# Optimization experiments

Measured on AMD Instinct MI355X. Metric: run time of the kernel, lower is better.

The kernel has to match this reference:

```python
import jax, jax.numpy as jnp
import numpy as np

D = 8  # polynomial degree; with bias present, basis has D columns (P1..PD)


def setup_inputs() -> dict:
    key = jax.random.key(0)
    k1, k2 = jax.random.split(key)
    batch, n_in, n_out = 65536, 256, 64
    x = jax.random.normal(k1, (batch, n_in), dtype=jnp.float32)
    c_basis = jax.random.normal(k2, (n_out, n_in, D), dtype=jnp.float32) * (1.0 / np.sqrt(n_in * D))
    bias = jnp.zeros((n_out,), dtype=jnp.float32)
    return {"x": x, "c_basis": c_basis, "bias": bias}


def _legendre_basis(x):
    # x: (batch, n_in). Returns (batch, n_in, D) = [P1(t), ..., PD(t)], t = tanh(x).
    t = jnp.tanh(x)
    p_prev = jnp.ones_like(t)  # P0
    p_curr = t                 # P1
    polys = [p_curr]
    for k in range(2, D + 1):  # small fixed-length loop over degree
        p_next = ((2 * k - 1) * t * p_curr - (k - 1) * p_prev) / k
        polys.append(p_next)
        p_prev, p_curr = p_curr, p_next
    return jnp.stack(polys, axis=-1)  # (batch, n_in, D)


def reference(x, c_basis, bias):
    # basis: (batch, n_in, D); contract over (n_in, D) with c_basis (n_out, n_in, D)
    leg = _legendre_basis(x)
    y = jnp.einsum('bid,oid->bo', leg, c_basis)
    return y + bias
```

## Files before the change

kernel.cpp:

```cpp
#include <hip/hip_runtime.h>
#include <hip/hip_bf16.h>

typedef _Float16 half2v __attribute__((ext_vector_type(2)));
typedef _Float16 half8  __attribute__((ext_vector_type(8)));
typedef __attribute__((ext_vector_type(4))) float floatx4;
typedef __attribute__((ext_vector_type(4))) unsigned int uintx4;

#define GLOBAL_AS __attribute__((address_space(1)))
#define LDS_AS __attribute__((address_space(3)))

__device__ __forceinline__ void async_ld16(const void* g, void* l) {
  __builtin_amdgcn_global_load_lds((const GLOBAL_AS unsigned int*)g,
                                   (LDS_AS unsigned int*)l, 16, 0, 0);
}

__device__ __forceinline__ half2v h2(float v) {
  return (half2v){(_Float16)v, (_Float16)v};
}

__device__ __forceinline__ void legendre2_f16(float xv0, float xv1,
                                              half8* fa0, half8* fa1) {
  float e0 = __builtin_amdgcn_exp2f(xv0 * 2.885390081777927f);
  float t0 = 1.0f - 2.0f * __builtin_amdgcn_rcpf(e0 + 1.0f);
  float e1 = __builtin_amdgcn_exp2f(xv1 * 2.885390081777927f);
  float t1 = 1.0f - 2.0f * __builtin_amdgcn_rcpf(e1 + 1.0f);
  half2v t;
  { auto tt = __builtin_amdgcn_cvt_pkrtz(t0, t1); __builtin_memcpy(&t, &tt, 4); }
  half2v p1 = t;
  half2v u2 = t * p1, w2 = u2 - h2(1.0f);  half2v p2 = h2(0.5f)      * w2 + u2;
  half2v u3 = t * p2, w3 = u3 - p1;        half2v p3 = h2(2.0f/3.0f) * w3 + u3;
  half2v u4 = t * p3, w4 = u4 - p2;        half2v p4 = h2(0.75f)     * w4 + u4;
  half2v u5 = t * p4, w5 = u5 - p3;        half2v p5 = h2(0.8f)      * w5 + u5;
  half2v u6 = t * p5, w6 = u6 - p4;        half2v p6 = h2(5.0f/6.0f) * w6 + u6;
  half2v u7 = t * p6, w7 = u7 - p5;        half2v p7 = h2(6.0f/7.0f) * w7 + u7;
  half2v u8 = t * p7, w8 = u8 - p6;        half2v p8 = h2(7.0f/8.0f) * w8 + u8;
  unsigned P[8];
  __builtin_memcpy(&P[0], &p1, 4); __builtin_memcpy(&P[1], &p2, 4);
  __builtin_memcpy(&P[2], &p3, 4); __builtin_memcpy(&P[3], &p4, 4);
  __builtin_memcpy(&P[4], &p5, 4); __builtin_memcpy(&P[5], &p6, 4);
  __builtin_memcpy(&P[6], &p7, 4); __builtin_memcpy(&P[7], &p8, 4);
  union { unsigned u[4]; half8 h; } a0, a1;
#pragma unroll
  for (int j = 0; j < 4; ++j) {
    a0.u[j] = __builtin_amdgcn_perm(P[2*j+1], P[2*j], 0x05040100u);
    a1.u[j] = __builtin_amdgcn_perm(P[2*j+1], P[2*j], 0x07060302u);
  }
  *fa0 = a0.h;
  *fa1 = a1.h;
}

__global__ void conv_kernel(const float* __restrict__ cb, _Float16* __restrict__ ws) {
  int t = blockIdx.x * 128 + threadIdx.x;
  int o = t >> 8;
  int i = t & 255;
  const floatx4* s = (const floatx4*)(cb + ((size_t)o * 256 + i) * 8);
  floatx4 v0 = s[0], v1 = s[1];
  union { _Float16 h[8]; uintx4 u; } w;
  w.h[0] = (_Float16)v0.x; w.h[1] = (_Float16)v0.y;
  w.h[2] = (_Float16)v0.z; w.h[3] = (_Float16)v0.w;
  w.h[4] = (_Float16)v1.x; w.h[5] = (_Float16)v1.y;
  w.h[6] = (_Float16)v1.z; w.h[7] = (_Float16)v1.w;
  *(uintx4*)(ws + (size_t)i * 512 + o * 8) = w.u;
}

#define MB 64
#define NCH 16

__global__ __launch_bounds__(128, 2) void kan_kernel(
    const float* __restrict__ x, const _Float16* __restrict__ ws,
    const float* __restrict__ bias, float* __restrict__ y) {
  __shared__ __align__(16) _Float16 bt[2][16 * 64 * 8];
  __shared__ __align__(16) float xs[2][MB * 16];

  const int tid  = threadIdx.x;
  const int wid  = tid >> 6;
  const int lane = tid & 63;
  const int m    = lane & 15;
  const int q    = lane >> 4;
  const int row_block = blockIdx.x * MB;

  floatx4 acc[2][4];
#pragma unroll
  for (int a = 0; a < 2; ++a)
#pragma unroll
    for (int nt = 0; nt < 4; ++nt) acc[a][nt] = (floatx4){0.f, 0.f, 0.f, 0.f};

  const _Float16* bsrc[8];
#pragma unroll
  for (int t = 0; t < 8; ++t)
    bsrc[t] = ws + (size_t)(t * 128 + wid * 64 + lane) * 8;
  const float* xsrc[2];
#pragma unroll
  for (int t = 0; t < 2; ++t) {
    int slot = t * 128 + wid * 64 + lane;
    int r = slot >> 2;
    int c4 = (slot & 3) ^ (r & 3);
    xsrc[t] = x + (size_t)(row_block + r) * 256 + c4 * 4;
  }

  auto stage = [&](int buf) {
#pragma unroll
    for (int t = 0; t < 8; ++t) {
      int sb = t * 128 + wid * 64;
      async_ld16(bsrc[t], &bt[buf][sb * 8]);
      bsrc[t] += 8192;
    }
#pragma unroll
    for (int t = 0; t < 2; ++t) {
      int sb = t * 128 + wid * 64;
      async_ld16(xsrc[t], &xs[buf][sb * 4]);
      xsrc[t] += 16;
    }
  };

  const int xoff0 = (wid * 32 + m) * 64 + ((m & 3) << 4) + q * 4;
  const int xoff1 = xoff0 + 1024;

  stage(0);
#pragma unroll 2
  for (int ch = 0; ch < NCH; ++ch) {
    const int buf = ch & 1;
    asm volatile("s_barrier" ::: "memory");
    if (ch + 1 < NCH) {
      stage(buf ^ 1);
      asm volatile("s_waitcnt vmcnt(10)" ::: "memory");
    } else {
      asm volatile("s_waitcnt vmcnt(0)" ::: "memory");
    }
    asm volatile("s_barrier" ::: "memory");

    const _Float16* bp = &bt[buf][q * 512 + m * 8];
    const char* xb = (const char*)&xs[buf][0];
#pragma unroll
    for (int ks = 0; ks < 4; ++ks) {
      half8 fb0 = *(const half8*)(bp + ks * 2048 + 0 * 128);
      half8 fb1 = *(const half8*)(bp + ks * 2048 + 1 * 128);
      half8 fb2 = *(const half8*)(bp + ks * 2048 + 2 * 128);
      half8 fb3 = *(const half8*)(bp + ks * 2048 + 3 * 128);
      float xv0 = *(const float*)(xb + (xoff0 ^ (ks << 4)));
      float xv1 = *(const float*)(xb + (xoff1 ^ (ks << 4)));
      half8 fa0, fa1;
      legendre2_f16(xv0, xv1, &fa0, &fa1);
      acc[0][0] = __builtin_amdgcn_mfma_f32_16x16x32_f16(fa0, fb0, acc[0][0], 0, 0, 0);
      acc[1][0] = __builtin_amdgcn_mfma_f32_16x16x32_f16(fa1, fb0, acc[1][0], 0, 0, 0);
      acc[0][1] = __builtin_amdgcn_mfma_f32_16x16x32_f16(fa0, fb1, acc[0][1], 0, 0, 0);
      acc[1][1] = __builtin_amdgcn_mfma_f32_16x16x32_f16(fa1, fb1, acc[1][1], 0, 0, 0);
      acc[0][2] = __builtin_amdgcn_mfma_f32_16x16x32_f16(fa0, fb2, acc[0][2], 0, 0, 0);
      acc[1][2] = __builtin_amdgcn_mfma_f32_16x16x32_f16(fa1, fb2, acc[1][2], 0, 0, 0);
      acc[0][3] = __builtin_amdgcn_mfma_f32_16x16x32_f16(fa0, fb3, acc[0][3], 0, 0, 0);
      acc[1][3] = __builtin_amdgcn_mfma_f32_16x16x32_f16(fa1, fb3, acc[1][3], 0, 0, 0);
    }
  }

  float bv[4];
#pragma unroll
  for (int nt = 0; nt < 4; ++nt) bv[nt] = bias[nt * 16 + m];
#pragma unroll
  for (int a = 0; a < 2; ++a) {
    int gr0 = row_block + wid * 32 + a * 16 + q * 4;
#pragma unroll
    for (int nt = 0; nt < 4; ++nt) {
#pragma unroll
      for (int r = 0; r < 4; ++r) {
        y[(size_t)(gr0 + r) * 64 + nt * 16 + m] = acc[a][nt][r] + bv[nt];
      }
    }
  }
}

extern "C" void kernel_launch(void* const* d_in, const int* in_sizes, int n_in,
                              void* d_out, int out_size, void* d_ws, size_t ws_size,
                              hipStream_t stream) {
  const float* x    = (const float*)d_in[0];
  const float* cb   = (const float*)d_in[1];
  const float* bias = (const float*)d_in[2];
  float* y = (float*)d_out;
  _Float16* ws = (_Float16*)d_ws;
  int batch = in_sizes[0] / 256;
  hipLaunchKernelGGL(conv_kernel, dim3(128), dim3(128), 0, stream, cb, ws);
  hipLaunchKernelGGL(kan_kernel, dim3(batch / MB), dim3(128), 0, stream, x, ws, bias, y);
}
```

Measured before the change: 120.4 us.

## Use four waves per block with one 16-row tile each

Moves the block from 2 waves covering 32 rows each to 4 waves covering 16 rows each. Each wave now computes the Legendre basis for one x value per lane using scalar fp16 math instead of packed half2 over two rows, and issues 4 MFMAs per k-step instead of 8. Staging loads are spread over 256 threads, and the vmcnt wait is adjusted to match. This aims for more waves in flight and lower per-wave register pressure, at the cost of losing the packed-fp16 ALU throughput and halving B-fragment reuse per LDS read.

```diff
diff --git a/kernel.cpp b/kernel.cpp
--- a/kernel.cpp
+++ b/kernel.cpp
@@ -18,35 +18,19 @@
   return (half2v){(_Float16)v, (_Float16)v};
 }
 
-__device__ __forceinline__ void legendre2_f16(float xv0, float xv1,
-                                              half8* fa0, half8* fa1) {
-  float e0 = __builtin_amdgcn_exp2f(xv0 * 2.885390081777927f);
-  float t0 = 1.0f - 2.0f * __builtin_amdgcn_rcpf(e0 + 1.0f);
-  float e1 = __builtin_amdgcn_exp2f(xv1 * 2.885390081777927f);
-  float t1 = 1.0f - 2.0f * __builtin_amdgcn_rcpf(e1 + 1.0f);
-  half2v t;
-  { auto tt = __builtin_amdgcn_cvt_pkrtz(t0, t1); __builtin_memcpy(&t, &tt, 4); }
-  half2v p1 = t;
-  half2v u2 = t * p1, w2 = u2 - h2(1.0f);  half2v p2 = h2(0.5f)      * w2 + u2;
-  half2v u3 = t * p2, w3 = u3 - p1;        half2v p3 = h2(2.0f/3.0f) * w3 + u3;
-  half2v u4 = t * p3, w4 = u4 - p2;        half2v p4 = h2(0.75f)     * w4 + u4;
-  half2v u5 = t * p4, w5 = u5 - p3;        half2v p5 = h2(0.8f)      * w5 + u5;
-  half2v u6 = t * p5, w6 = u6 - p4;        half2v p6 = h2(5.0f/6.0f) * w6 + u6;
-  half2v u7 = t * p6, w7 = u7 - p5;        half2v p7 = h2(6.0f/7.0f) * w7 + u7;
-  half2v u8 = t * p7, w8 = u8 - p6;        half2v p8 = h2(7.0f/8.0f) * w8 + u8;
-  unsigned P[8];
-  __builtin_memcpy(&P[0], &p1, 4); __builtin_memcpy(&P[1], &p2, 4);
-  __builtin_memcpy(&P[2], &p3, 4); __builtin_memcpy(&P[3], &p4, 4);
-  __builtin_memcpy(&P[4], &p5, 4); __builtin_memcpy(&P[5], &p6, 4);
-  __builtin_memcpy(&P[6], &p7, 4); __builtin_memcpy(&P[7], &p8, 4);
-  union { unsigned u[4]; half8 h; } a0, a1;
-#pragma unroll
-  for (int j = 0; j < 4; ++j) {
-    a0.u[j] = __builtin_amdgcn_perm(P[2*j+1], P[2*j], 0x05040100u);
-    a1.u[j] = __builtin_amdgcn_perm(P[2*j+1], P[2*j], 0x07060302u);
-  }
-  *fa0 = a0.h;
-  *fa1 = a1.h;
+__device__ __forceinline__ half8 legendre_f16(float xv) {
+  float e = __builtin_amdgcn_exp2f(xv * 2.885390081777927f);
+  float t0 = 1.0f - 2.0f * __builtin_amdgcn_rcpf(e + 1.0f);
+  _Float16 t = (_Float16)t0;
+  _Float16 p1 = t;
+  _Float16 u2 = t * p1, w2 = u2 - (_Float16)1.0f; _Float16 p2 = (_Float16)(0.5f)      * w2 + u2;
+  _Float16 u3 = t * p2, w3 = u3 - p1;             _Float16 p3 = (_Float16)(2.0f/3.0f) * w3 + u3;
+  _Float16 u4 = t * p3, w4 = u4 - p2;             _Float16 p4 = (_Float16)(0.75f)     * w4 + u4;
+  _Float16 u5 = t * p4, w5 = u5 - p3;             _Float16 p5 = (_Float16)(0.8f)      * w5 + u5;
+  _Float16 u6 = t * p5, w6 = u6 - p4;             _Float16 p6 = (_Float16)(5.0f/6.0f) * w6 + u6;
+  _Float16 u7 = t * p6, w7 = u7 - p5;             _Float16 p7 = (_Float16)(6.0f/7.0f) * w7 + u7;
+  _Float16 u8 = t * p7, w8 = u8 - p6;             _Float16 p8 = (_Float16)(7.0f/8.0f) * w8 + u8;
+  return (half8){p1, p2, p3, p4, p5, p6, p7, p8};
 }
 
 __global__ void conv_kernel(const float* __restrict__ cb, _Float16* __restrict__ ws) {
@@ -66,7 +50,7 @@
 #define MB 64
 #define NCH 16
 
-__global__ __launch_bounds__(128, 2) void kan_kernel(
+__global__ __launch_bounds__(256, 4) void kan_kernel(
     const float* __restrict__ x, const _Float16* __restrict__ ws,
     const float* __restrict__ bias, float* __restrict__ y) {
   __shared__ __align__(16) _Float16 bt[2][16 * 64 * 8];
@@ -79,42 +63,34 @@
   const int q    = lane >> 4;
   const int row_block = blockIdx.x * MB;
 
-  floatx4 acc[2][4];
+  floatx4 acc[4];
 #pragma unroll
-  for (int a = 0; a < 2; ++a)
+  for (int nt = 0; nt < 4; ++nt) acc[nt] = (floatx4){0.f, 0.f, 0.f, 0.f};
+
+  const _Float16* bsrc[4];
 #pragma unroll
-    for (int nt = 0; nt < 4; ++nt) acc[a][nt] = (floatx4){0.f, 0.f, 0.f, 0.f};
-
-  const _Float16* bsrc[8];
-#pragma unroll
-  for (int t = 0; t < 8; ++t)
-    bsrc[t] = ws + (size_t)(t * 128 + wid * 64 + lane) * 8;
-  const float* xsrc[2];
-#pragma unroll
-  for (int t = 0; t < 2; ++t) {
-    int slot = t * 128 + wid * 64 + lane;
+  for (int t = 0; t < 4; ++t)
+    bsrc[t] = ws + (size_t)(t * 256 + wid * 64 + lane) * 8;
+  const float* xsrc;
+  {
+    int slot = wid * 64 + lane;
     int r = slot >> 2;
     int c4 = (slot & 3) ^ (r & 3);
-    xsrc[t] = x + (size_t)(row_block + r) * 256 + c4 * 4;
+    xsrc = x + (size_t)(row_block + r) * 256 + c4 * 4;
   }
 
   auto stage = [&](int buf) {
 #pragma unroll
-    for (int t = 0; t < 8; ++t) {
-      int sb = t * 128 + wid * 64;
+    for (int t = 0; t < 4; ++t) {
+      int sb = t * 256 + wid * 64;
       async_ld16(bsrc[t], &bt[buf][sb * 8]);
       bsrc[t] += 8192;
     }
-#pragma unroll
-    for (int t = 0; t < 2; ++t) {
-      int sb = t * 128 + wid * 64;
-      async_ld16(xsrc[t], &xs[buf][sb * 4]);
-      xsrc[t] += 16;
-    }
+    async_ld16(xsrc, &xs[buf][(wid * 64) * 4]);
+    xsrc += 16;
   };
 
-  const int xoff0 = (wid * 32 + m) * 64 + ((m & 3) << 4) + q * 4;
-  const int xoff1 = xoff0 + 1024;
+  const int xoff = (wid * 16 + m) * 64 + ((m & 3) << 4) + q * 4;
 
   stage(0);
 #pragma unroll 2
@@ -123,7 +99,7 @@
     asm volatile("s_barrier" ::: "memory");
     if (ch + 1 < NCH) {
       stage(buf ^ 1);
-      asm volatile("s_waitcnt vmcnt(10)" ::: "memory");
+      asm volatile("s_waitcnt vmcnt(5)" ::: "memory");
     } else {
       asm volatile("s_waitcnt vmcnt(0)" ::: "memory");
     }
@@ -137,33 +113,24 @@
       half8 fb1 = *(const half8*)(bp + ks * 2048 + 1 * 128);
       half8 fb2 = *(const half8*)(bp + ks * 2048 + 2 * 128);
       half8 fb3 = *(const half8*)(bp + ks * 2048 + 3 * 128);
-      float xv0 = *(const float*)(xb + (xoff0 ^ (ks << 4)));
-      float xv1 = *(const float*)(xb + (xoff1 ^ (ks << 4)));
-      half8 fa0, fa1;
-      legendre2_f16(xv0, xv1, &fa0, &fa1);
-      acc[0][0] = __builtin_amdgcn_mfma_f32_16x16x32_f16(fa0, fb0, acc[0][0], 0, 0, 0);
-      acc[1][0] = __builtin_amdgcn_mfma_f32_16x16x32_f16(fa1, fb0, acc[1][0], 0, 0, 0);
-      acc[0][1] = __builtin_amdgcn_mfma_f32_16x16x32_f16(fa0, fb1, acc[0][1], 0, 0, 0);
-      acc[1][1] = __builtin_amdgcn_mfma_f32_16x16x32_f16(fa1, fb1, acc[1][1], 0, 0, 0);
-      acc[0][2] = __builtin_amdgcn_mfma_f32_16x16x32_f16(fa0, fb2, acc[0][2], 0, 0, 0);
-      acc[1][2] = __builtin_amdgcn_mfma_f32_16x16x32_f16(fa1, fb2, acc[1][2], 0, 0, 0);
-      acc[0][3] = __builtin_amdgcn_mfma_f32_16x16x32_f16(fa0, fb3, acc[0][3], 0, 0, 0);
-      acc[1][3] = __builtin_amdgcn_mfma_f32_16x16x32_f16(fa1, fb3, acc[1][3], 0, 0, 0);
+      float xv = *(const float*)(xb + (xoff ^ (ks << 4)));
+      half8 fa = legendre_f16(xv);
+      acc[0] = __builtin_amdgcn_mfma_f32_16x16x32_f16(fa, fb0, acc[0], 0, 0, 0);
+      acc[1] = __builtin_amdgcn_mfma_f32_16x16x32_f16(fa, fb1, acc[1], 0, 0, 0);
+      acc[2] = __builtin_amdgcn_mfma_f32_16x16x32_f16(fa, fb2, acc[2], 0, 0, 0);
+      acc[3] = __builtin_amdgcn_mfma_f32_16x16x32_f16(fa, fb3, acc[3], 0, 0, 0);
     }
   }
 
   float bv[4];
 #pragma unroll
   for (int nt = 0; nt < 4; ++nt) bv[nt] = bias[nt * 16 + m];
+  int gr0 = row_block + wid * 16 + q * 4;
 #pragma unroll
-  for (int a = 0; a < 2; ++a) {
-    int gr0 = row_block + wid * 32 + a * 16 + q * 4;
+  for (int nt = 0; nt < 4; ++nt) {
 #pragma unroll
-    for (int nt = 0; nt < 4; ++nt) {
-#pragma unroll
-      for (int r = 0; r < 4; ++r) {
-        y[(size_t)(gr0 + r) * 64 + nt * 16 + m] = acc[a][nt][r] + bv[nt];
-      }
+    for (int r = 0; r < 4; ++r) {
+      y[(size_t)(gr0 + r) * 64 + nt * 16 + m] = acc[nt][r] + bv[nt];
     }
   }
 }
@@ -178,5 +145,5 @@
   _Float16* ws = (_Float16*)d_ws;
   int batch = in_sizes[0] / 256;
   hipLaunchKernelGGL(conv_kernel, dim3(128), dim3(128), 0, stream, cb, ws);
-  hipLaunchKernelGGL(kan_kernel, dim3(batch / MB), dim3(128), 0, stream, x, ws, bias, y);
+  hipLaunchKernelGGL(kan_kernel, dim3(batch / MB), dim3(256), 0, stream, x, ws, bias, y);
 }
```

New measurement: 125.1 us. +3.9%, slower.

## Split K across waves with register-prefetched direct loads instead of LDS staging

Applied to the files above, without the earlier changes.

Replaces the LDS double-buffered async staging with direct global loads into registers, software-prefetched one or two iterations ahead. The two waves in a block now split the 256-wide input dimension, each covering 32 rows, and their partial sums are combined through shared memory at the end. This drops the per-chunk barriers, doubles the grid size and raises the occupancy hint to 4. In exchange, each wave reads the weights straight from global or L2, with some redundancy across blocks, and x is read with scalar strided loads.

```diff
diff --git a/kernel.cpp b/kernel.cpp
--- a/kernel.cpp
+++ b/kernel.cpp
@@ -6,13 +6,7 @@
 typedef __attribute__((ext_vector_type(4))) float floatx4;
 typedef __attribute__((ext_vector_type(4))) unsigned int uintx4;
 
-#define GLOBAL_AS __attribute__((address_space(1)))
-#define LDS_AS __attribute__((address_space(3)))
-
-__device__ __forceinline__ void async_ld16(const void* g, void* l) {
-  __builtin_amdgcn_global_load_lds((const GLOBAL_AS unsigned int*)g,
-                                   (LDS_AS unsigned int*)l, 16, 0, 0);
-}
+#define SCHED_FENCE() asm volatile("" ::: "memory")
 
 __device__ __forceinline__ half2v h2(float v) {
   return (half2v){(_Float16)v, (_Float16)v};
@@ -63,21 +57,19 @@
   *(uintx4*)(ws + (size_t)i * 512 + o * 8) = w.u;
 }
 
-#define MB 64
-#define NCH 16
+#define ITERS 32
 
-__global__ __launch_bounds__(128, 2) void kan_kernel(
+__global__ __launch_bounds__(128, 4) void kan_kernel(
     const float* __restrict__ x, const _Float16* __restrict__ ws,
     const float* __restrict__ bias, float* __restrict__ y) {
-  __shared__ __align__(16) _Float16 bt[2][16 * 64 * 8];
-  __shared__ __align__(16) float xs[2][MB * 16];
+  __shared__ floatx4 red[8 * 64];
 
   const int tid  = threadIdx.x;
   const int wid  = tid >> 6;
   const int lane = tid & 63;
   const int m    = lane & 15;
   const int q    = lane >> 4;
-  const int row_block = blockIdx.x * MB;
+  const int row_block = blockIdx.x * 32;
 
   floatx4 acc[2][4];
 #pragma unroll
@@ -85,84 +77,66 @@
 #pragma unroll
     for (int nt = 0; nt < 4; ++nt) acc[a][nt] = (floatx4){0.f, 0.f, 0.f, 0.f};
 
-  const _Float16* bsrc[8];
+  const float* xp0 = x + (size_t)(row_block + m) * 256 + wid * 128 + q;
+  const float* xp1 = xp0 + 16 * 256;
+  const _Float16* bp = ws + (size_t)wid * 65536 + q * 512 + m * 8;
+
+  float xq0[4], xq1[4];
+  half8 fbq[2][4];
+  xq0[0] = xp0[0]; xq1[0] = xp1[0];
+  xq0[1] = xp0[4]; xq1[1] = xp1[4];
 #pragma unroll
-  for (int t = 0; t < 8; ++t)
-    bsrc[t] = ws + (size_t)(t * 128 + wid * 64 + lane) * 8;
-  const float* xsrc[2];
+  for (int nt = 0; nt < 4; ++nt) fbq[0][nt] = *(const half8*)(bp + nt * 128);
+  SCHED_FENCE();
+
 #pragma unroll
-  for (int t = 0; t < 2; ++t) {
-    int slot = t * 128 + wid * 64 + lane;
-    int r = slot >> 2;
-    int c4 = (slot & 3) ^ (r & 3);
-    xsrc[t] = x + (size_t)(row_block + r) * 256 + c4 * 4;
+  for (int s = 0; s < ITERS; ++s) {
+    if (s + 2 < ITERS) {
+      xq0[(s + 2) & 3] = xp0[(s + 2) * 4];
+      xq1[(s + 2) & 3] = xp1[(s + 2) * 4];
+    }
+    if (s + 1 < ITERS) {
+#pragma unroll
+      for (int nt = 0; nt < 4; ++nt)
+        fbq[(s + 1) & 1][nt] = *(const half8*)(bp + (size_t)(s + 1) * 2048 + nt * 128);
+    }
+    SCHED_FENCE();
+
+    half8 fa0, fa1;
+    legendre2_f16(xq0[s & 3], xq1[s & 3], &fa0, &fa1);
+    const int b = s & 1;
+    acc[0][0] = __builtin_amdgcn_mfma_f32_16x16x32_f16(fa0, fbq[b][0], acc[0][0], 0, 0, 0);
+    acc[1][0] = __builtin_amdgcn_mfma_f32_16x16x32_f16(fa1, fbq[b][0], acc[1][0], 0, 0, 0);
+    acc[0][1] = __builtin_amdgcn_mfma_f32_16x16x32_f16(fa0, fbq[b][1], acc[0][1], 0, 0, 0);
+    acc[1][1] = __builtin_amdgcn_mfma_f32_16x16x32_f16(fa1, fbq[b][1], acc[1][1], 0, 0, 0);
+    acc[0][2] = __builtin_amdgcn_mfma_f32_16x16x32_f16(fa0, fbq[b][2], acc[0][2], 0, 0, 0);
+    acc[1][2] = __builtin_amdgcn_mfma_f32_16x16x32_f16(fa1, fbq[b][2], acc[1][2], 0, 0, 0);
+    acc[0][3] = __builtin_amdgcn_mfma_f32_16x16x32_f16(fa0, fbq[b][3], acc[0][3], 0, 0, 0);
+    acc[1][3] = __builtin_amdgcn_mfma_f32_16x16x32_f16(fa1, fbq[b][3], acc[1][3], 0, 0, 0);
   }
 
-  auto stage = [&](int buf) {
+  if (wid == 1) {
 #pragma unroll
-    for (int t = 0; t < 8; ++t) {
-      int sb = t * 128 + wid * 64;
-      async_ld16(bsrc[t], &bt[buf][sb * 8]);
-      bsrc[t] += 8192;
-    }
+    for (int a = 0; a < 2; ++a)
 #pragma unroll
-    for (int t = 0; t < 2; ++t) {
-      int sb = t * 128 + wid * 64;
-      async_ld16(xsrc[t], &xs[buf][sb * 4]);
-      xsrc[t] += 16;
-    }
-  };
-
-  const int xoff0 = (wid * 32 + m) * 64 + ((m & 3) << 4) + q * 4;
-  const int xoff1 = xoff0 + 1024;
-
-  stage(0);
-#pragma unroll 2
-  for (int ch = 0; ch < NCH; ++ch) {
-    const int buf = ch & 1;
-    asm volatile("s_barrier" ::: "memory");
-    if (ch + 1 < NCH) {
-      stage(buf ^ 1);
-      asm volatile("s_waitcnt vmcnt(10)" ::: "memory");
-    } else {
-      asm volatile("s_waitcnt vmcnt(0)" ::: "memory");
-    }
-    asm volatile("s_barrier" ::: "memory");
-
-    const _Float16* bp = &bt[buf][q * 512 + m * 8];
-    const char* xb = (const char*)&xs[buf][0];
+      for (int nt = 0; nt < 4; ++nt)
+        red[(a * 4 + nt) * 64 + lane] = acc[a][nt];
+  }
+  __syncthreads();
+  if (wid == 0) {
+    float bv[4];
 #pragma unroll
-    for (int ks = 0; ks < 4; ++ks) {
-      half8 fb0 = *(const half8*)(bp + ks * 2048 + 0 * 128);
-      half8 fb1 = *(const half8*)(bp + ks * 2048 + 1 * 128);
-      half8 fb2 = *(const half8*)(bp + ks * 2048 + 2 * 128);
-      half8 fb3 = *(const half8*)(bp + ks * 2048 + 3 * 128);
-      float xv0 = *(const float*)(xb + (xoff0 ^ (ks << 4)));
-      float xv1 = *(const float*)(xb + (xoff1 ^ (ks << 4)));
-      half8 fa0, fa1;
-      legendre2_f16(xv0, xv1, &fa0, &fa1);
-      acc[0][0] = __builtin_amdgcn_mfma_f32_16x16x32_f16(fa0, fb0, acc[0][0], 0, 0, 0);
-      acc[1][0] = __builtin_amdgcn_mfma_f32_16x16x32_f16(fa1, fb0, acc[1][0], 0, 0, 0);
-      acc[0][1] = __builtin_amdgcn_mfma_f32_16x16x32_f16(fa0, fb1, acc[0][1], 0, 0, 0);
-      acc[1][1] = __builtin_amdgcn_mfma_f32_16x16x32_f16(fa1, fb1, acc[1][1], 0, 0, 0);
-      acc[0][2] = __builtin_amdgcn_mfma_f32_16x16x32_f16(fa0, fb2, acc[0][2], 0, 0, 0);
-      acc[1][2] = __builtin_amdgcn_mfma_f32_16x16x32_f16(fa1, fb2, acc[1][2], 0, 0, 0);
-      acc[0][3] = __builtin_amdgcn_mfma_f32_16x16x32_f16(fa0, fb3, acc[0][3], 0, 0, 0);
-      acc[1][3] = __builtin_amdgcn_mfma_f32_16x16x32_f16(fa1, fb3, acc[1][3], 0, 0, 0);
-    }
-  }
-
-  float bv[4];
+    for (int nt = 0; nt < 4; ++nt) bv[nt] = bias[nt * 16 + m];
 #pragma unroll
-  for (int nt = 0; nt < 4; ++nt) bv[nt] = bias[nt * 16 + m];
+    for (int a = 0; a < 2; ++a) {
+      int gr0 = row_block + a * 16 + q * 4;
 #pragma unroll
-  for (int a = 0; a < 2; ++a) {
-    int gr0 = row_block + wid * 32 + a * 16 + q * 4;
+      for (int nt = 0; nt < 4; ++nt) {
+        floatx4 p = red[(a * 4 + nt) * 64 + lane];
 #pragma unroll
-    for (int nt = 0; nt < 4; ++nt) {
-#pragma unroll
-      for (int r = 0; r < 4; ++r) {
-        y[(size_t)(gr0 + r) * 64 + nt * 16 + m] = acc[a][nt][r] + bv[nt];
+        for (int r = 0; r < 4; ++r) {
+          y[(size_t)(gr0 + r) * 64 + nt * 16 + m] = acc[a][nt][r] + p[r] + bv[nt];
+        }
       }
     }
   }
@@ -178,5 +152,5 @@
   _Float16* ws = (_Float16*)d_ws;
   int batch = in_sizes[0] / 256;
   hipLaunchKernelGGL(conv_kernel, dim3(128), dim3(128), 0, stream, cb, ws);
-  hipLaunchKernelGGL(kan_kernel, dim3(batch / MB), dim3(128), 0, stream, x, ws, bias, y);
+  hipLaunchKernelGGL(kan_kernel, dim3(batch / 32), dim3(128), 0, stream, x, ws, bias, y);
 }
```

Measured after the change: 141.6 us. 17.6% more time.
